# Kernel tuning notes

Measured on AMD Instinct MI355X. Metric: run time of the kernel, lower is better.

Reference implementation:

```python
import jax, jax.numpy as jnp
import numpy as np

DIM = 256
NUM_HEADS = 8
HEAD_DIM = DIM // NUM_HEADS


def setup_inputs() -> dict:
    key = jax.random.key(0)
    k_x, k_wq, k_bq, k_wp, k_bp = jax.random.split(key, 5)
    B, C, H, W = 2, DIM, 48, 48
    x = jax.random.normal(k_x, (B, C, H, W), dtype=jnp.float32)
    # 1x1 convs are pointwise matmuls: store weights as [out, in]
    w_qkv = jax.random.normal(k_wq, (3 * C, C), dtype=jnp.float32) * (1.0 / np.sqrt(C))
    b_qkv = jax.random.normal(k_bq, (3 * C,), dtype=jnp.float32) * 0.01
    w_proj = jax.random.normal(k_wp, (C, C), dtype=jnp.float32) * (1.0 / np.sqrt(C))
    b_proj = jax.random.normal(k_bp, (C,), dtype=jnp.float32) * 0.01
    return {"x": x, "w_qkv": w_qkv, "b_qkv": b_qkv, "w_proj": w_proj, "b_proj": b_proj}


def reference(x, w_qkv, b_qkv, w_proj, b_proj):
    B, C, H, W = x.shape
    N = H * W
    # qkv 1x1 conv -> pointwise channel matmul
    qkv = jnp.einsum('bchw,oc->bohw', x, w_qkv) + b_qkv[None, :, None, None]
    q, k, v = jnp.split(qkv, 3, axis=1)  # each [B, C, H, W]
    q = q.reshape(B, NUM_HEADS, HEAD_DIM, N)
    k = k.reshape(B, NUM_HEADS, HEAD_DIM, N)
    v = v.reshape(B, NUM_HEADS, HEAD_DIM, N)
    scale = 1.0 / (HEAD_DIM ** 0.5)
    attn = jnp.einsum('bhdn,bhdm->bhnm', q, k) * scale  # [B, H, N, N]
    attn = jax.nn.softmax(attn, axis=-1)
    out = jnp.einsum('bhnm,bhdm->bhdn', attn, v)  # [B, heads, head_dim, N]
    out = out.reshape(B, C, H, W)
    out = jnp.einsum('bchw,oc->bohw', out, w_proj) + b_proj[None, :, None, None]
    return out + x
```

## Files before the change

### kernel.cpp

```cpp
#include <hip/hip_runtime.h>
#include <math.h>

#define C_DIM 256
#define NH 8
#define HD 32
#define BATCH 2
#define NPIX 2304
#define TK 64
#define NGRP (NPIX / 16)

typedef __attribute__((ext_vector_type(8))) short bf16x8;
typedef __attribute__((ext_vector_type(4))) float f32x4;

#define OFF_XT  0u
#define OFF_Q   1179648u
#define OFF_K   2359296u
#define OFF_V   3538944u
#define OFF_OT  4718592u
#define OFF_WQ  5898240u
#define OFF_WP  6094848u

__device__ __forceinline__ unsigned short f2b(float f) {
    union { float f; unsigned int u; } c; c.f = f;
    unsigned int u = c.u + 0x7FFFu + ((c.u >> 16) & 1u);
    return (unsigned short)(u >> 16);
}
__device__ __forceinline__ unsigned int pk2(float lo, float hi) {
    union { float f; unsigned int u; } a, b;
    a.f = lo; b.f = hi;
    return __builtin_amdgcn_perm(b.u + 0x8000u, a.u + 0x8000u, 0x07060302u);
}

__global__ __launch_bounds__(256) void prep_xt(
        const float* __restrict__ x, unsigned short* __restrict__ xT)
{
    __shared__ unsigned short t_s[64][72];
    const int tid = threadIdx.x;
    const int n0 = blockIdx.x * 64, c0 = blockIdx.y * 64, b = blockIdx.z;
    const int nl = tid & 63, cq = tid >> 6;
    #pragma unroll
    for (int p = 0; p < 8; ++p) {
        const int c = p * 8 + cq * 2;
        const float f0 = x[((size_t)b * C_DIM + c0 + c) * NPIX + n0 + nl];
        const float f1 = x[((size_t)b * C_DIM + c0 + c + 1) * NPIX + n0 + nl];
        *(unsigned int*)&t_s[nl][c] = pk2(f0, f1);
    }
    __syncthreads();
    const int row = tid >> 2, jq = tid & 3;
    #pragma unroll
    for (int hh = 0; hh < 2; ++hh) {
        const int jl = jq * 2 + hh;
        const int jg = blockIdx.y * 8 + jl;
        const int ngrp = blockIdx.x * 4 + (row >> 4);
        unsigned short* dst = xT + (((size_t)b * NGRP + ngrp) * 32 + jg) * 128 + (row & 15) * 8;
        *(uint4*)dst = *(uint4*)&t_s[row][jl * 8];
    }
}

__global__ __launch_bounds__(256) void prep_w(
        const float* __restrict__ wqkv, const float* __restrict__ wproj,
        unsigned short* __restrict__ wq, unsigned short* __restrict__ wp)
{
    const int t = blockIdx.x * 256 + threadIdx.x;
    const float* src; unsigned short* dst;
    if (t < 24576) {
        const int m = t >> 5, j = t & 31;
        src = wqkv + ((size_t)m * C_DIM + j * 8);
        dst = wq + ((size_t)((m >> 4) * 32 + j) * 16 + (m & 15)) * 8;
    } else {
        const int t2 = t - 24576, m = t2 >> 5, j = t2 & 31;
        src = wproj + ((size_t)m * C_DIM + j * 8);
        dst = wp + ((size_t)((m >> 4) * 32 + j) * 16 + (m & 15)) * 8;
    }
    const float4 f0 = *(const float4*)src, f1 = *(const float4*)(src + 4);
    *(uint4*)dst = make_uint4(pk2(f0.x, f0.y), pk2(f0.z, f0.w),
                              pk2(f1.x, f1.y), pk2(f1.z, f1.w));
}

__global__ __launch_bounds__(256) void qkv_gemm(
        const unsigned short* __restrict__ xT, const unsigned short* __restrict__ wq,
        const float* __restrict__ bias,
        unsigned short* __restrict__ Qg, unsigned short* __restrict__ Kg,
        unsigned short* __restrict__ Vg)
{
    __shared__ unsigned short eplds[4][2560];
    const int tid = threadIdx.x, wv = tid >> 6, lane = tid & 63;
    const int l15 = lane & 15, quad = lane >> 4;
    const int n0 = blockIdx.x * 256, my = blockIdx.y, b = blockIdx.z;
    const int nw = n0 + wv * 64;

    bf16x8 af[8];
    #pragma unroll
    for (int kc = 0; kc < 8; ++kc)
        af[kc] = *(const bf16x8*)(wq + ((size_t)(my * 32 + kc * 4 + quad) * 16 + l15) * 8);

    f32x4 acc[4];
    #pragma unroll
    for (int i = 0; i < 4; ++i) acc[i] = (f32x4){0.f, 0.f, 0.f, 0.f};

    #pragma unroll
    for (int sub = 0; sub < 4; ++sub) {
        const int ngrp = (nw + sub * 16) >> 4;
        const unsigned short* bp = xT + ((size_t)b * NGRP + ngrp) * 32 * 128;
        #pragma unroll
        for (int kc = 0; kc < 8; ++kc) {
            const bf16x8 bf = *(const bf16x8*)(bp + (size_t)(kc * 4 + quad) * 128 + l15 * 8);
            acc[sub] = __builtin_amdgcn_mfma_f32_16x16x32_bf16(af[kc], bf, acc[sub], 0, 0, 0);
        }
    }

    const int which = my >> 4;
    const int ch0 = (my & 15) * 16;
    const int h = ch0 >> 5, d0 = ch0 & 31, bh = b * NH + h;
    const float4 b4 = *(const float4*)(bias + my * 16 + quad * 4);
    unsigned short* wl = eplds[wv];

    if (which < 2) {
        const float sc = (which == 0) ? 0.17677669529663687f : 1.0f;
        #pragma unroll
        for (int sub = 0; sub < 4; ++sub) {
            const float v0 = (acc[sub][0] + b4.x) * sc, v1 = (acc[sub][1] + b4.y) * sc;
            const float v2 = (acc[sub][2] + b4.z) * sc, v3 = (acc[sub][3] + b4.w) * sc;
            *(uint2*)&wl[(sub * 16 + l15) * 40 + quad * 4] =
                make_uint2(pk2(v0, v1), pk2(v2, v3));
        }
        unsigned short* dst = ((which == 0) ? Qg : Kg)
                            + ((size_t)bh * NPIX + nw + lane) * HD + d0;
        *(uint4*)dst       = *(uint4*)&wl[lane * 40];
        *(uint4*)(dst + 8) = *(uint4*)&wl[lane * 40 + 8];
    } else {
        #pragma unroll
        for (int sub = 0; sub < 4; ++sub) {
            wl[(quad * 4 + 0) * 72 + sub * 16 + l15] = f2b(acc[sub][0] + b4.x);
            wl[(quad * 4 + 1) * 72 + sub * 16 + l15] = f2b(acc[sub][1] + b4.y);
            wl[(quad * 4 + 2) * 72 + sub * 16 + l15] = f2b(acc[sub][2] + b4.z);
            wl[(quad * 4 + 3) * 72 + sub * 16 + l15] = f2b(acc[sub][3] + b4.w);
        }
        #pragma unroll
        for (int p = 0; p < 2; ++p) {
            const int row = p * 8 + (lane >> 3), cn = (lane & 7) * 8;
            *(uint4*)(Vg + ((size_t)bh * HD + d0 + row) * NPIX + nw + cn) =
                *(uint4*)&wl[row * 72 + cn];
        }
    }
}

#define NT (NPIX / TK)

__global__ __launch_bounds__(256) void attn_kernel(
        const unsigned short* __restrict__ Qg, const unsigned short* __restrict__ Kg,
        const unsigned short* __restrict__ Vg, unsigned short* __restrict__ OtT)
{
    __shared__ unsigned short k_s[2][TK][40];
    __shared__ unsigned short v_s[2][HD][76];
    __shared__ unsigned short p_s[4][16][76];
    __shared__ unsigned short o_sT[64][40];

    const int tid  = threadIdx.x;
    const int wv   = tid >> 6;
    const int lane = tid & 63;
    const int l15  = lane & 15;
    const int quad = lane >> 4;
    const int bh   = blockIdx.x;
    const int q0   = blockIdx.y * 64;

    const unsigned short* Qh = Qg + (size_t)bh * NPIX * HD;
    const unsigned short* Kh = Kg + (size_t)bh * NPIX * HD;
    const unsigned short* Vh = Vg + (size_t)bh * HD * NPIX;

    const bf16x8 q_frag = *(const bf16x8*)(Qh + (size_t)(q0 + wv * 16 + l15) * HD + quad * 8);

    const int kr = tid >> 2, kc = (tid & 3) * 8;
    const int vd = tid >> 3, vc = (tid & 7) * 8;

    uint4 kreg = *(const uint4*)(Kh + (size_t)kr * HD + kc);
    uint4 vreg = *(const uint4*)(Vh + (size_t)vd * NPIX + vc);
    *(uint4*)&k_s[0][kr][kc] = kreg;
    *(uint4*)&v_s[0][vd][vc] = vreg;

    f32x4 o0 = {0.f, 0.f, 0.f, 0.f};
    f32x4 o1 = {0.f, 0.f, 0.f, 0.f};
    float lsum = 0.f;

    for (int t = 0; t < NT; ++t) {
        const int cur = t & 1;
        if (t + 1 < NT) {
            const int k0 = (t + 1) * TK;
            kreg = *(const uint4*)(Kh + (size_t)(k0 + kr) * HD + kc);
            vreg = *(const uint4*)(Vh + (size_t)vd * NPIX + k0 + vc);
        }
        __syncthreads();

        f32x4 s[4];
        #pragma unroll
        for (int kg = 0; kg < 4; ++kg) {
            const bf16x8 kf = *(const bf16x8*)&k_s[cur][kg * 16 + l15][quad * 8];
            s[kg] = __builtin_amdgcn_mfma_f32_16x16x32_bf16(kf, q_frag,
                        (f32x4){0.f, 0.f, 0.f, 0.f}, 0, 0, 0);
        }

        #pragma unroll
        for (int kg = 0; kg < 4; ++kg) {
            const float p0 = __expf(s[kg][0]);
            const float p1 = __expf(s[kg][1]);
            const float p2 = __expf(s[kg][2]);
            const float p3 = __expf(s[kg][3]);
            lsum += (p0 + p1) + (p2 + p3);
            *(uint2*)&p_s[wv][l15][kg * 16 + quad * 4] =
                make_uint2(pk2(p0, p1), pk2(p2, p3));
        }

        #pragma unroll
        for (int kc2 = 0; kc2 < 2; ++kc2) {
            const bf16x8 pf  = *(const bf16x8*)&p_s[wv][l15][kc2 * 32 + quad * 8];
            const bf16x8 vf0 = *(const bf16x8*)&v_s[cur][l15][kc2 * 32 + quad * 8];
            const bf16x8 vf1 = *(const bf16x8*)&v_s[cur][16 + l15][kc2 * 32 + quad * 8];
            o0 = __builtin_amdgcn_mfma_f32_16x16x32_bf16(vf0, pf, o0, 0, 0, 0);
            o1 = __builtin_amdgcn_mfma_f32_16x16x32_bf16(vf1, pf, o1, 0, 0, 0);
        }

        if (t + 1 < NT) {
            *(uint4*)&k_s[cur ^ 1][kr][kc] = kreg;
            *(uint4*)&v_s[cur ^ 1][vd][vc] = vreg;
        }
    }

    lsum += __shfl_xor(lsum, 16, 64);
    lsum += __shfl_xor(lsum, 32, 64);
    const float inv = 1.f / lsum;

    *(uint2*)&o_sT[wv * 16 + l15][quad * 4] =
        make_uint2(pk2(o0[0] * inv, o0[1] * inv), pk2(o0[2] * inv, o0[3] * inv));
    *(uint2*)&o_sT[wv * 16 + l15][16 + quad * 4] =
        make_uint2(pk2(o1[0] * inv, o1[1] * inv), pk2(o1[2] * inv, o1[3] * inv));
    __syncthreads();
    const int row = tid >> 2, jq = tid & 3;
    const int b = bh >> 3, h = bh & 7;
    const int q = q0 + row;
    unsigned short* dst = OtT + (((size_t)b * NGRP + (q >> 4)) * 32 + h * 4 + jq) * 128
                        + (q & 15) * 8;
    *(uint4*)dst = *(uint4*)&o_sT[row][jq * 8];
}

__global__ __launch_bounds__(256) void proj_gemm(
        const unsigned short* __restrict__ OtT, const unsigned short* __restrict__ wp,
        const float* __restrict__ bias, const float* __restrict__ x,
        float* __restrict__ out)
{
    __shared__ float plds[4][576];
    const int tid = threadIdx.x, wv = tid >> 6, lane = tid & 63;
    const int l15 = lane & 15, quad = lane >> 4;
    const int n0 = blockIdx.x * 128, my = blockIdx.y, b = blockIdx.z;
    const int nw = n0 + wv * 32;

    bf16x8 af[8];
    #pragma unroll
    for (int kc = 0; kc < 8; ++kc)
        af[kc] = *(const bf16x8*)(wp + ((size_t)(my * 32 + kc * 4 + quad) * 16 + l15) * 8);

    f32x4 acc[2];
    acc[0] = (f32x4){0.f, 0.f, 0.f, 0.f};
    acc[1] = (f32x4){0.f, 0.f, 0.f, 0.f};

    #pragma unroll
    for (int sub = 0; sub < 2; ++sub) {
        const int ngrp = (nw + sub * 16) >> 4;
        const unsigned short* bp = OtT + ((size_t)b * NGRP + ngrp) * 32 * 128;
        #pragma unroll
        for (int kc = 0; kc < 8; ++kc) {
            const bf16x8 bf = *(const bf16x8*)(bp + (size_t)(kc * 4 + quad) * 128 + l15 * 8);
            acc[sub] = __builtin_amdgcn_mfma_f32_16x16x32_bf16(af[kc], bf, acc[sub], 0, 0, 0);
        }
    }

    float* wl = plds[wv];
    #pragma unroll
    for (int sub = 0; sub < 2; ++sub) {
        wl[(quad * 4 + 0) * 36 + sub * 16 + l15] = acc[sub][0];
        wl[(quad * 4 + 1) * 36 + sub * 16 + l15] = acc[sub][1];
        wl[(quad * 4 + 2) * 36 + sub * 16 + l15] = acc[sub][2];
        wl[(quad * 4 + 3) * 36 + sub * 16 + l15] = acc[sub][3];
    }
    const int m0 = my * 16;
    #pragma unroll
    for (int p = 0; p < 2; ++p) {
        const int row = p * 8 + (lane >> 3), cn = (lane & 7) * 4;
        const int c = m0 + row;
        const size_t idx = ((size_t)b * C_DIM + c) * NPIX + nw + cn;
        const f32x4 v = *(const f32x4*)&wl[row * 36 + cn];
        const f32x4 r = *(const f32x4*)(x + idx);
        const float bv = bias[c];
        f32x4 o;
        o[0] = v[0] + bv + r[0]; o[1] = v[1] + bv + r[1];
        o[2] = v[2] + bv + r[2]; o[3] = v[3] + bv + r[3];
        *(f32x4*)(out + idx) = o;
    }
}

extern "C" void kernel_launch(void* const* d_in, const int* in_sizes, int n_in,
                              void* d_out, int out_size, void* d_ws, size_t ws_size,
                              hipStream_t stream)
{
    const float* x      = (const float*)d_in[0];
    const float* w_qkv  = (const float*)d_in[1];
    const float* b_qkv  = (const float*)d_in[2];
    const float* w_proj = (const float*)d_in[3];
    const float* b_proj = (const float*)d_in[4];
    float* out = (float*)d_out;

    unsigned short* ws = (unsigned short*)d_ws;
    unsigned short* xT  = ws + OFF_XT;
    unsigned short* Qg  = ws + OFF_Q;
    unsigned short* Kg  = ws + OFF_K;
    unsigned short* Vg  = ws + OFF_V;
    unsigned short* OtT = ws + OFF_OT;
    unsigned short* wq  = ws + OFF_WQ;
    unsigned short* wp  = ws + OFF_WP;

    prep_xt<<<dim3(36, 4, 2), 256, 0, stream>>>(x, xT);
    prep_w<<<dim3(128), 256, 0, stream>>>(w_qkv, w_proj, wq, wp);
    qkv_gemm<<<dim3(9, 48, 2), 256, 0, stream>>>(xT, wq, b_qkv, Qg, Kg, Vg);
    attn_kernel<<<dim3(16, 36), 256, 0, stream>>>(Qg, Kg, Vg, OtT);
    proj_gemm<<<dim3(18, 16, 2), 256, 0, stream>>>(OtT, wp, b_proj, x, out);
}
```

Baseline: 120.8 us.

## Split attention over key range with fp32 partials and add normalization kernel

The attention kernel now splits the key dimension into two halves (grid z=2). Each block writes unnormalized fp32 partial outputs and row sums, and a new norm_kernel combines them, normalizes, and packs the result to bf16 in the layout proj_gemm expects. This doubles the block count from 576 to 1152 to fill the GPU better, at the cost of extra global traffic and an additional launch. The QKV GEMM also computes two 16-row M tiles per block, so each block covers a full head's 32 channels with wider stores. Launch bounds now carry occupancy hints. The split skips a running max, which is safe only because the scores are already unscaled-safe in the original as well.

```diff
diff --git a/kernel.cpp b/kernel.cpp
--- a/kernel.cpp
+++ b/kernel.cpp
@@ -8,6 +8,7 @@
 #define NPIX 2304
 #define TK 64
 #define NGRP (NPIX / 16)
+#define TPB 18
 
 typedef __attribute__((ext_vector_type(8))) short bf16x8;
 typedef __attribute__((ext_vector_type(4))) float f32x4;
@@ -19,6 +20,7 @@
 #define OFF_OT  4718592u
 #define OFF_WQ  5898240u
 #define OFF_WP  6094848u
+#define OFF_F32 6160384u
 
 __device__ __forceinline__ unsigned short f2b(float f) {
     union { float f; unsigned int u; } c; c.f = f;
@@ -77,7 +79,7 @@
                               pk2(f1.x, f1.y), pk2(f1.z, f1.w));
 }
 
-__global__ __launch_bounds__(256) void qkv_gemm(
+__global__ __launch_bounds__(256, 2) void qkv_gemm(
         const unsigned short* __restrict__ xT, const unsigned short* __restrict__ wq,
         const float* __restrict__ bias,
         unsigned short* __restrict__ Qg, unsigned short* __restrict__ Kg,
@@ -89,14 +91,19 @@
     const int n0 = blockIdx.x * 256, my = blockIdx.y, b = blockIdx.z;
     const int nw = n0 + wv * 64;
 
-    bf16x8 af[8];
-    #pragma unroll
-    for (int kc = 0; kc < 8; ++kc)
-        af[kc] = *(const bf16x8*)(wq + ((size_t)(my * 32 + kc * 4 + quad) * 16 + l15) * 8);
-
-    f32x4 acc[4];
-    #pragma unroll
-    for (int i = 0; i < 4; ++i) acc[i] = (f32x4){0.f, 0.f, 0.f, 0.f};
+    bf16x8 af[2][8];
+    #pragma unroll
+    for (int mt = 0; mt < 2; ++mt)
+        #pragma unroll
+        for (int kc = 0; kc < 8; ++kc)
+            af[mt][kc] = *(const bf16x8*)(wq +
+                ((size_t)((my * 2 + mt) * 32 + kc * 4 + quad) * 16 + l15) * 8);
+
+    f32x4 acc[2][4];
+    #pragma unroll
+    for (int mt = 0; mt < 2; ++mt)
+        #pragma unroll
+        for (int s = 0; s < 4; ++s) acc[mt][s] = (f32x4){0.f, 0.f, 0.f, 0.f};
 
     #pragma unroll
     for (int sub = 0; sub < 4; ++sub) {
@@ -105,56 +112,62 @@
         #pragma unroll
         for (int kc = 0; kc < 8; ++kc) {
             const bf16x8 bf = *(const bf16x8*)(bp + (size_t)(kc * 4 + quad) * 128 + l15 * 8);
-            acc[sub] = __builtin_amdgcn_mfma_f32_16x16x32_bf16(af[kc], bf, acc[sub], 0, 0, 0);
-        }
-    }
-
-    const int which = my >> 4;
-    const int ch0 = (my & 15) * 16;
-    const int h = ch0 >> 5, d0 = ch0 & 31, bh = b * NH + h;
-    const float4 b4 = *(const float4*)(bias + my * 16 + quad * 4);
+            acc[0][sub] = __builtin_amdgcn_mfma_f32_16x16x32_bf16(af[0][kc], bf, acc[0][sub], 0, 0, 0);
+            acc[1][sub] = __builtin_amdgcn_mfma_f32_16x16x32_bf16(af[1][kc], bf, acc[1][sub], 0, 0, 0);
+        }
+    }
+
+    const int which = my >> 3;
+    const int h = my & 7, bh = b * NH + h;
+    float4 b4[2];
+    b4[0] = *(const float4*)(bias + my * 32 + quad * 4);
+    b4[1] = *(const float4*)(bias + my * 32 + 16 + quad * 4);
     unsigned short* wl = eplds[wv];
 
     if (which < 2) {
         const float sc = (which == 0) ? 0.17677669529663687f : 1.0f;
         #pragma unroll
-        for (int sub = 0; sub < 4; ++sub) {
-            const float v0 = (acc[sub][0] + b4.x) * sc, v1 = (acc[sub][1] + b4.y) * sc;
-            const float v2 = (acc[sub][2] + b4.z) * sc, v3 = (acc[sub][3] + b4.w) * sc;
-            *(uint2*)&wl[(sub * 16 + l15) * 40 + quad * 4] =
-                make_uint2(pk2(v0, v1), pk2(v2, v3));
-        }
+        for (int mt = 0; mt < 2; ++mt)
+            #pragma unroll
+            for (int sub = 0; sub < 4; ++sub) {
+                const float v0 = (acc[mt][sub][0] + b4[mt].x) * sc;
+                const float v1 = (acc[mt][sub][1] + b4[mt].y) * sc;
+                const float v2 = (acc[mt][sub][2] + b4[mt].z) * sc;
+                const float v3 = (acc[mt][sub][3] + b4[mt].w) * sc;
+                *(uint2*)&wl[(sub * 16 + l15) * 40 + mt * 16 + quad * 4] =
+                    make_uint2(pk2(v0, v1), pk2(v2, v3));
+            }
         unsigned short* dst = ((which == 0) ? Qg : Kg)
-                            + ((size_t)bh * NPIX + nw + lane) * HD + d0;
-        *(uint4*)dst       = *(uint4*)&wl[lane * 40];
-        *(uint4*)(dst + 8) = *(uint4*)&wl[lane * 40 + 8];
+                            + ((size_t)bh * NPIX + nw + lane) * HD;
+        #pragma unroll
+        for (int i = 0; i < 4; ++i)
+            *((uint4*)dst + i) = *(uint4*)&wl[lane * 40 + i * 8];
     } else {
         #pragma unroll
-        for (int sub = 0; sub < 4; ++sub) {
-            wl[(quad * 4 + 0) * 72 + sub * 16 + l15] = f2b(acc[sub][0] + b4.x);
-            wl[(quad * 4 + 1) * 72 + sub * 16 + l15] = f2b(acc[sub][1] + b4.y);
-            wl[(quad * 4 + 2) * 72 + sub * 16 + l15] = f2b(acc[sub][2] + b4.z);
-            wl[(quad * 4 + 3) * 72 + sub * 16 + l15] = f2b(acc[sub][3] + b4.w);
-        }
-        #pragma unroll
-        for (int p = 0; p < 2; ++p) {
-            const int row = p * 8 + (lane >> 3), cn = (lane & 7) * 8;
-            *(uint4*)(Vg + ((size_t)bh * HD + d0 + row) * NPIX + nw + cn) =
-                *(uint4*)&wl[row * 72 + cn];
-        }
-    }
-}
-
-#define NT (NPIX / TK)
-
-__global__ __launch_bounds__(256) void attn_kernel(
+        for (int mt = 0; mt < 2; ++mt)
+            #pragma unroll
+            for (int sub = 0; sub < 4; ++sub) {
+                wl[(mt * 16 + quad * 4 + 0) * 72 + sub * 16 + l15] = f2b(acc[mt][sub][0] + b4[mt].x);
+                wl[(mt * 16 + quad * 4 + 1) * 72 + sub * 16 + l15] = f2b(acc[mt][sub][1] + b4[mt].y);
+                wl[(mt * 16 + quad * 4 + 2) * 72 + sub * 16 + l15] = f2b(acc[mt][sub][2] + b4[mt].z);
+                wl[(mt * 16 + quad * 4 + 3) * 72 + sub * 16 + l15] = f2b(acc[mt][sub][3] + b4[mt].w);
+            }
+        const int row = lane >> 1, seg = (lane & 1) * 32;
+        unsigned short* dst = Vg + ((size_t)bh * HD + row) * NPIX + nw + seg;
+        #pragma unroll
+        for (int i = 0; i < 4; ++i)
+            *((uint4*)dst + i) = *(uint4*)&wl[row * 72 + seg + i * 8];
+    }
+}
+
+__global__ __launch_bounds__(256, 4) void attn_kernel(
         const unsigned short* __restrict__ Qg, const unsigned short* __restrict__ Kg,
-        const unsigned short* __restrict__ Vg, unsigned short* __restrict__ OtT)
+        const unsigned short* __restrict__ Vg,
+        float* __restrict__ OtP, float* __restrict__ lsumP)
 {
     __shared__ unsigned short k_s[2][TK][40];
     __shared__ unsigned short v_s[2][HD][76];
     __shared__ unsigned short p_s[4][16][76];
-    __shared__ unsigned short o_sT[64][40];
 
     const int tid  = threadIdx.x;
     const int wv   = tid >> 6;
@@ -163,6 +176,8 @@
     const int quad = lane >> 4;
     const int bh   = blockIdx.x;
     const int q0   = blockIdx.y * 64;
+    const int sp   = blockIdx.z;
+    const int t0   = sp * TPB;
 
     const unsigned short* Qh = Qg + (size_t)bh * NPIX * HD;
     const unsigned short* Kh = Kg + (size_t)bh * NPIX * HD;
@@ -173,8 +188,8 @@
     const int kr = tid >> 2, kc = (tid & 3) * 8;
     const int vd = tid >> 3, vc = (tid & 7) * 8;
 
-    uint4 kreg = *(const uint4*)(Kh + (size_t)kr * HD + kc);
-    uint4 vreg = *(const uint4*)(Vh + (size_t)vd * NPIX + vc);
+    uint4 kreg = *(const uint4*)(Kh + (size_t)(t0 * TK + kr) * HD + kc);
+    uint4 vreg = *(const uint4*)(Vh + (size_t)vd * NPIX + t0 * TK + vc);
     *(uint4*)&k_s[0][kr][kc] = kreg;
     *(uint4*)&v_s[0][vd][vc] = vreg;
 
@@ -182,10 +197,10 @@
     f32x4 o1 = {0.f, 0.f, 0.f, 0.f};
     float lsum = 0.f;
 
-    for (int t = 0; t < NT; ++t) {
+    for (int t = 0; t < TPB; ++t) {
         const int cur = t & 1;
-        if (t + 1 < NT) {
-            const int k0 = (t + 1) * TK;
+        if (t + 1 < TPB) {
+            const int k0 = (t0 + t + 1) * TK;
             kreg = *(const uint4*)(Kh + (size_t)(k0 + kr) * HD + kc);
             vreg = *(const uint4*)(Vh + (size_t)vd * NPIX + k0 + vc);
         }
@@ -219,7 +234,7 @@
             o1 = __builtin_amdgcn_mfma_f32_16x16x32_bf16(vf1, pf, o1, 0, 0, 0);
         }
 
-        if (t + 1 < NT) {
+        if (t + 1 < TPB) {
             *(uint4*)&k_s[cur ^ 1][kr][kc] = kreg;
             *(uint4*)&v_s[cur ^ 1][vd][vc] = vreg;
         }
@@ -227,19 +242,49 @@
 
     lsum += __shfl_xor(lsum, 16, 64);
     lsum += __shfl_xor(lsum, 32, 64);
-    const float inv = 1.f / lsum;
-
-    *(uint2*)&o_sT[wv * 16 + l15][quad * 4] =
-        make_uint2(pk2(o0[0] * inv, o0[1] * inv), pk2(o0[2] * inv, o0[3] * inv));
-    *(uint2*)&o_sT[wv * 16 + l15][16 + quad * 4] =
-        make_uint2(pk2(o1[0] * inv, o1[1] * inv), pk2(o1[2] * inv, o1[3] * inv));
+
     __syncthreads();
-    const int row = tid >> 2, jq = tid & 3;
+    float* pp = (float*)&p_s[wv][0][0];
+    #pragma unroll
+    for (int r = 0; r < 4; ++r) {
+        pp[l15 * 36 + quad * 4 + r]      = o0[r];
+        pp[l15 * 36 + 16 + quad * 4 + r] = o1[r];
+    }
+    if (quad == 0)
+        lsumP[((size_t)sp * 16 + bh) * NPIX + q0 + wv * 16 + l15] = lsum;
+    __syncthreads();
+    const int q = lane >> 2, off = (lane & 3) * 8;
+    float* dst = OtP + (((size_t)sp * 16 + bh) * NPIX + q0 + wv * 16 + q) * 32 + off;
+    *(float4*)dst       = *(float4*)&pp[q * 36 + off];
+    *((float4*)dst + 1) = *(float4*)&pp[q * 36 + off + 4];
+}
+
+__global__ __launch_bounds__(256) void norm_kernel(
+        const float* __restrict__ OtP, const float* __restrict__ lsumP,
+        unsigned short* __restrict__ OtT)
+{
+    const int q = blockIdx.x * 256 + threadIdx.x;
+    const int bh = blockIdx.y;
+    const float* pa = OtP + ((size_t)bh * NPIX + q) * 32;
+    const float* pb = OtP + ((size_t)(16 + bh) * NPIX + q) * 32;
+    const float inv = 1.f / (lsumP[(size_t)bh * NPIX + q] +
+                             lsumP[(size_t)(16 + bh) * NPIX + q]);
     const int b = bh >> 3, h = bh & 7;
-    const int q = q0 + row;
-    unsigned short* dst = OtT + (((size_t)b * NGRP + (q >> 4)) * 32 + h * 4 + jq) * 128
-                        + (q & 15) * 8;
-    *(uint4*)dst = *(uint4*)&o_sT[row][jq * 8];
+    unsigned short* cell = OtT + (((size_t)b * NGRP + (q >> 4)) * 32 + h * 4) * 128
+                         + (q & 15) * 8;
+    #pragma unroll
+    for (int jq = 0; jq < 4; ++jq) {
+        const float4 a0 = *(const float4*)(pa + jq * 8);
+        const float4 a1 = *(const float4*)(pa + jq * 8 + 4);
+        const float4 b0 = *(const float4*)(pb + jq * 8);
+        const float4 b1 = *(const float4*)(pb + jq * 8 + 4);
+        const float o0 = (a0.x + b0.x) * inv, o1 = (a0.y + b0.y) * inv;
+        const float o2 = (a0.z + b0.z) * inv, o3 = (a0.w + b0.w) * inv;
+        const float o4 = (a1.x + b1.x) * inv, o5 = (a1.y + b1.y) * inv;
+        const float o6 = (a1.z + b1.z) * inv, o7 = (a1.w + b1.w) * inv;
+        *(uint4*)(cell + jq * 128) = make_uint4(pk2(o0, o1), pk2(o2, o3),
+                                                pk2(o4, o5), pk2(o6, o7));
+    }
 }
 
 __global__ __launch_bounds__(256) void proj_gemm(
@@ -316,10 +361,14 @@
     unsigned short* OtT = ws + OFF_OT;
     unsigned short* wq  = ws + OFF_WQ;
     unsigned short* wp  = ws + OFF_WP;
+    float* fws   = (float*)(ws + OFF_F32);
+    float* OtP   = fws;
+    float* lsumP = fws + 4718592;
 
     prep_xt<<<dim3(36, 4, 2), 256, 0, stream>>>(x, xT);
     prep_w<<<dim3(128), 256, 0, stream>>>(w_qkv, w_proj, wq, wp);
-    qkv_gemm<<<dim3(9, 48, 2), 256, 0, stream>>>(xT, wq, b_qkv, Qg, Kg, Vg);
-    attn_kernel<<<dim3(16, 36), 256, 0, stream>>>(Qg, Kg, Vg, OtT);
+    qkv_gemm<<<dim3(9, 24, 2), 256, 0, stream>>>(xT, wq, b_qkv, Qg, Kg, Vg);
+    attn_kernel<<<dim3(16, 36, 2), 256, 0, stream>>>(Qg, Kg, Vg, OtP, lsumP);
+    norm_kernel<<<dim3(9, 16), 256, 0, stream>>>(OtP, lsumP, OtT);
     proj_gemm<<<dim3(18, 16, 2), 256, 0, stream>>>(OtT, wp, b_proj, x, out);
 }
```

Result: faster. 117.9 us (-2.4%).
